# Kernel tuning notes

Hardware: AMD Instinct MI355X
Metric: run time of the kernel (lower is better)

## Reference

```python
import jax, jax.numpy as jnp
import numpy as np

ALPHA = 32.0
LN_EPS = 1e-5

def _cdist(a, b):
    # a: [C, M, K], b: [C, N, K] -> [C, M, N] euclidean distances
    d2 = (jnp.sum(a * a, -1)[:, :, None]
          + jnp.sum(b * b, -1)[:, None, :]
          - 2.0 * jnp.einsum('cmk,cnk->cmn', a, b))
    return jnp.sqrt(jnp.maximum(d2, 1e-12))

def setup_inputs() -> dict:
    key = jax.random.key(0)
    k1, k2 = jax.random.split(key)
    B, D, H, W, C = 8, 16, 28, 28, 256
    CN, SS = 128, 28 * 28
    x = jax.random.normal(k1, (B, D, H, W, C), dtype=jnp.float32)
    ln_weight = jnp.ones((C,), dtype=jnp.float32)
    ln_bias = jnp.zeros((C,), dtype=jnp.float32)
    cluster_center = jax.random.uniform(k2, (C, CN, SS), dtype=jnp.float32)
    return {"x": x, "ln_weight": ln_weight, "ln_bias": ln_bias,
            "cluster_center": cluster_center}

def reference(x, ln_weight, ln_bias, cluster_center):
    B, D, H, W, C = x.shape
    CN = cluster_center.shape[1]
    # LayerNorm over last dim (feature_dim)
    mu = jnp.mean(x, -1, keepdims=True)
    var = jnp.mean(jnp.square(x - mu), -1, keepdims=True)
    xn = (x - mu) * jax.lax.rsqrt(var + LN_EPS) * ln_weight + ln_bias
    # B D H W C -> C (B D) (H W)
    x_re = jnp.transpose(xn, (4, 0, 1, 2, 3)).reshape(C, B * D, H * W)
    soft_assign = _cdist(x_re, cluster_center)          # [C, B*D, CN]
    # C (B D) CN -> B D C CN
    x_distance = jnp.transpose(soft_assign.reshape(C, B, D, CN), (1, 2, 0, 3))
    # NegSoftAssign: exp(-alpha*(x - min)) normalized == softmax(-alpha*x)
    x_distance_assign = jax.nn.softmax(-ALPHA * x_distance, axis=-1)
    cluster_dist = _cdist(cluster_center, cluster_center)  # [C, CN, CN]
    return (x_distance, x_distance_assign, cluster_dist)
```

## Files before the change

### kernel.cpp

```cpp
#include <hip/hip_runtime.h>
#include <hip/hip_bf16.h>
#include <math.h>

#define C_DIM 256
#define BD    128
#define HW    784
#define CN    128
#define KPAD  832
#define KTILES 26

typedef short bf16x8 __attribute__((ext_vector_type(8)));
typedef float f32x4 __attribute__((ext_vector_type(4)));

__device__ inline ushort f2b(float f) {
  unsigned u = __float_as_uint(f);
  unsigned r = (u + 0x7FFFu + ((u >> 16) & 1u)) >> 16;
  return (ushort)r;
}

__global__ __launch_bounds__(256) void ln_transpose_kernel(
    const float* __restrict__ x, const float* __restrict__ lnw,
    const float* __restrict__ lnb, ushort* __restrict__ xre,
    float* __restrict__ anorm) {
  __shared__ ushort btile[256 * 64];
  __shared__ float nbuf[4][256];
  const int t = threadIdx.x, bd = blockIdx.y, bx = blockIdx.x;
  const int hw0 = bx * 64;
  const int w = t >> 6, lane = t & 63;
  const int q = lane >> 4, l = lane & 15;
  const bool last = (bx == 12);
  const int ngroups = last ? 1 : 4;
  const int rpw = ngroups * 4;
  if (last) {
    for (int r = 16; r < 64; r += 4)
      *(ushort4*)&btile[t * 64 + r] = make_ushort4(0, 0, 0, 0);
  }
  float4 wv[4], bv[4];
  for (int s = 0; s < 4; ++s) {
    wv[s] = *(const float4*)(lnw + s * 64 + l * 4);
    bv[s] = *(const float4*)(lnb + s * 64 + l * 4);
  }
  float nrm[4][4];
  for (int s = 0; s < 4; ++s)
    for (int j = 0; j < 4; ++j) nrm[s][j] = 0.f;
  const float* xb = x + ((size_t)bd * HW + hw0) * 256 + l * 4;
  const int xr = l & 12;
  for (int g = 0; g < ngroups; ++g) {
    int r = w * rpw + g * 4 + q;
    float4 v[4];
    for (int s = 0; s < 4; ++s)
      v[s] = *(const float4*)(xb + (size_t)r * 256 + s * 64);
    float sum = 0.f, sq = 0.f;
    for (int s = 0; s < 4; ++s) {
      sum += v[s].x + v[s].y + v[s].z + v[s].w;
      sq = fmaf(v[s].x, v[s].x, sq); sq = fmaf(v[s].y, v[s].y, sq);
      sq = fmaf(v[s].z, v[s].z, sq); sq = fmaf(v[s].w, v[s].w, sq);
    }
    for (int off = 1; off <= 8; off <<= 1) {
      sum += __shfl_xor(sum, off, 64);
      sq  += __shfl_xor(sq, off, 64);
    }
    float mu = sum * (1.f / 256.f);
    float var = fmaf(-mu, mu, sq * (1.f / 256.f));
    float sc = rsqrtf(var + 1e-5f);
    int rp = r ^ xr;
    for (int s = 0; s < 4; ++s) {
      float y0 = (v[s].x - mu) * sc * wv[s].x + bv[s].x;
      float y1 = (v[s].y - mu) * sc * wv[s].y + bv[s].y;
      float y2 = (v[s].z - mu) * sc * wv[s].z + bv[s].z;
      float y3 = (v[s].w - mu) * sc * wv[s].w + bv[s].w;
      nrm[s][0] = fmaf(y0, y0, nrm[s][0]);
      nrm[s][1] = fmaf(y1, y1, nrm[s][1]);
      nrm[s][2] = fmaf(y2, y2, nrm[s][2]);
      nrm[s][3] = fmaf(y3, y3, nrm[s][3]);
      int c = s * 64 + l * 4;
      btile[(c + 0) * 64 + rp] = f2b(y0);
      btile[(c + 1) * 64 + rp] = f2b(y1);
      btile[(c + 2) * 64 + rp] = f2b(y2);
      btile[(c + 3) * 64 + rp] = f2b(y3);
    }
  }
  for (int s = 0; s < 4; ++s)
    for (int j = 0; j < 4; ++j) {
      float v = nrm[s][j];
      v += __shfl_xor(v, 16, 64);
      v += __shfl_xor(v, 32, 64);
      nrm[s][j] = v;
    }
  if (q == 0)
    for (int s = 0; s < 4; ++s)
      for (int j = 0; j < 4; ++j) nbuf[w][s * 64 + l * 4 + j] = nrm[s][j];
  __syncthreads();
  float tot = nbuf[0][t] + nbuf[1][t] + nbuf[2][t] + nbuf[3][t];
  atomicAdd(&anorm[t * 128 + bd], tot);
  for (int i = 0; i < 16; ++i) {
    int c = w * 64 + i * 4 + (lane >> 4);
    int xw = (w * 16 + i) & 12;
    int ho = (lane & 15) * 4;
    uint2 val = *(const uint2*)&btile[c * 64 + (ho ^ xw)];
    *(uint2*)(xre + (size_t)c * (BD * KPAD) + (size_t)bd * KPAD + hw0 + ho) = val;
  }
}

__global__ __launch_bounds__(256) void cc_convert_kernel(
    const float* __restrict__ cc, ushort* __restrict__ ccb,
    float* __restrict__ bnorm) {
  int b = blockIdx.x, c = b >> 3;
  int t = threadIdx.x, w = t >> 6, lane = t & 63;
  int q = lane >> 4, l = lane & 15;
  int r = (b & 7) * 16 + w * 4 + q;
  const float4* src = (const float4*)(cc + ((size_t)c * CN + r) * HW);
  ushort* dst = ccb + ((size_t)c * CN + r) * KPAD;
  float nrm = 0.f;
  for (int i = 0; i < 13; ++i) {
    int f = i * 16 + l;
    if (f < 196) {
      float4 v = src[f];
      nrm = fmaf(v.x, v.x, nrm); nrm = fmaf(v.y, v.y, nrm);
      nrm = fmaf(v.z, v.z, nrm); nrm = fmaf(v.w, v.w, nrm);
      ushort4 o; o.x = f2b(v.x); o.y = f2b(v.y); o.z = f2b(v.z); o.w = f2b(v.w);
      *(ushort4*)(dst + f * 4) = o;
    }
  }
  for (int off = 1; off <= 8; off <<= 1) nrm += __shfl_xor(nrm, off, 64);
  if (l == 0) bnorm[c * 128 + r] = nrm;
  if (l < 12) *(ushort4*)(dst + 784 + l * 4) = make_ushort4(0, 0, 0, 0);
}

__global__ __launch_bounds__(256, 4) void gemm_mfma_kernel(
    const ushort* __restrict__ xre, const ushort* __restrict__ ccb,
    const float* __restrict__ anorm, const float* __restrict__ bnorm,
    float* __restrict__ out_d, float* __restrict__ out_c) {
  __shared__ __align__(16) ushort At[2][4096];
  __shared__ __align__(16) ushort Bt[2][2048];
  const int bx = blockIdx.x;
  const int c = bx >> 2, mode = (bx >> 1) & 1, nh = bx & 1;
  const int t = threadIdx.x, w = t >> 6, lane = t & 63;
  const int quad = lane >> 4, ln = lane & 15;
  const ushort* Ag = (mode ? ccb : xre) + (size_t)c * (128 * KPAD);
  const ushort* Bg = ccb + (size_t)c * (128 * KPAD) + (size_t)(nh * 64) * KPAD;

  f32x4 acc[2][4];
  for (int i = 0; i < 2; ++i)
    for (int j = 0; j < 4; ++j) acc[i][j] = f32x4{0.f, 0.f, 0.f, 0.f};

  const int ciA0 = w * 128 + lane, ciA1 = ciA0 + 64;
  const int rowA0 = ciA0 >> 2, rowA1 = ciA1 >> 2;
  const int qA0 = (ciA0 & 3) ^ (rowA0 & 3), qA1 = (ciA1 & 3) ^ (rowA1 & 3);
  const ushort* gA0 = Ag + (size_t)rowA0 * KPAD + qA0 * 8;
  const ushort* gA1 = Ag + (size_t)rowA1 * KPAD + qA1 * 8;
  const int rowB = t >> 2, qB = (t & 3) ^ (rowB & 3);
  const ushort* gB = Bg + (size_t)rowB * KPAD + qB * 8;

#define ISSUE(k, p)                                                            \
  do {                                                                         \
    int kb = (k) * 32;                                                         \
    __builtin_amdgcn_global_load_lds(                                          \
        (const __attribute__((address_space(1))) unsigned int*)(gA0 + kb),     \
        (__attribute__((address_space(3))) unsigned int*)&At[p][ciA0 * 8], 16, 0, 0); \
    __builtin_amdgcn_global_load_lds(                                          \
        (const __attribute__((address_space(1))) unsigned int*)(gA1 + kb),     \
        (__attribute__((address_space(3))) unsigned int*)&At[p][ciA1 * 8], 16, 0, 0); \
    if (!mode)                                                                 \
      __builtin_amdgcn_global_load_lds(                                        \
          (const __attribute__((address_space(1))) unsigned int*)(gB + kb),    \
          (__attribute__((address_space(3))) unsigned int*)&Bt[p][t * 8], 16, 0, 0); \
  } while (0)

  ISSUE(0, 0);
  for (int k0 = 0; k0 < KTILES; ++k0) {
    __syncthreads();
    if (k0 < KTILES - 1) ISSUE(k0 + 1, (k0 + 1) & 1);
    const int p = k0 & 1;
    const ushort* Ab = At[p];
    bf16x8 af[2], bf[4];
    for (int i = 0; i < 2; ++i) {
      int m = w * 32 + i * 16 + ln;
      af[i] = *(const bf16x8*)&Ab[(m * 4 + (quad ^ (m & 3))) * 8];
    }
    for (int j = 0; j < 4; ++j) {
      int n = j * 16 + ln;
      if (mode) {
        int mr = nh * 64 + n;
        bf[j] = *(const bf16x8*)&Ab[(mr * 4 + (quad ^ (mr & 3))) * 8];
      } else {
        bf[j] = *(const bf16x8*)&Bt[p][(n * 4 + (quad ^ (n & 3))) * 8];
      }
    }
    for (int i = 0; i < 2; ++i)
      for (int j = 0; j < 4; ++j)
        acc[i][j] = __builtin_amdgcn_mfma_f32_16x16x32_bf16(af[i], bf[j], acc[i][j], 0, 0, 0);
  }
#undef ISSUE

  const float* rn = (mode ? bnorm : anorm) + c * 128;
  const float* cnp = bnorm + c * 128 + nh * 64;
  float cnv[4];
  for (int j = 0; j < 4; ++j) cnv[j] = cnp[j * 16 + ln];
  for (int i = 0; i < 2; ++i) {
    float rv[4];
    for (int r = 0; r < 4; ++r) rv[r] = rn[w * 32 + i * 16 + quad * 4 + r];
    for (int r = 0; r < 4; ++r) {
      int m = w * 32 + i * 16 + quad * 4 + r;
      float dr[4];
      for (int j = 0; j < 4; ++j) {
        float d2 = rv[r] + cnv[j] - 2.f * acc[i][j][r];
        dr[j] = sqrtf(fmaxf(d2, 1e-12f));
      }
      if (mode) {
        float* ob = out_c + (size_t)c * (128 * 128) + (size_t)m * 128 + nh * 64;
        for (int j = 0; j < 4; ++j) ob[j * 16 + ln] = dr[j];
      } else {
        float* ob = out_d + ((size_t)m * 256 + c) * 128 + nh * 64;
        for (int j = 0; j < 4; ++j) ob[j * 16 + ln] = dr[j];
      }
    }
  }
}

__global__ __launch_bounds__(256) void softmax_kernel(
    const float* __restrict__ out_d, float* __restrict__ out_s) {
  const int t = threadIdx.x, w = t >> 6, lane = t & 63;
  const int q = lane >> 4, l = lane & 15;
  const int row = blockIdx.x * 16 + w * 4 + q;
  const float4* src = (const float4*)(out_d + (size_t)row * 128);
  float4 v0 = src[l], v1 = src[l + 16];
  float mn = fminf(fminf(fminf(v0.x, v0.y), fminf(v0.z, v0.w)),
                   fminf(fminf(v1.x, v1.y), fminf(v1.z, v1.w)));
  for (int off = 1; off <= 8; off <<= 1) mn = fminf(mn, __shfl_xor(mn, off, 64));
  float e[8];
  e[0] = __expf(-32.f * (v0.x - mn)); e[1] = __expf(-32.f * (v0.y - mn));
  e[2] = __expf(-32.f * (v0.z - mn)); e[3] = __expf(-32.f * (v0.w - mn));
  e[4] = __expf(-32.f * (v1.x - mn)); e[5] = __expf(-32.f * (v1.y - mn));
  e[6] = __expf(-32.f * (v1.z - mn)); e[7] = __expf(-32.f * (v1.w - mn));
  float s = e[0] + e[1] + e[2] + e[3] + e[4] + e[5] + e[6] + e[7];
  for (int off = 1; off <= 8; off <<= 1) s += __shfl_xor(s, off, 64);
  float inv = 1.f / s;
  float4* dst = (float4*)(out_s + (size_t)row * 128);
  dst[l]      = make_float4(e[0] * inv, e[1] * inv, e[2] * inv, e[3] * inv);
  dst[l + 16] = make_float4(e[4] * inv, e[5] * inv, e[6] * inv, e[7] * inv);
}

extern "C" void kernel_launch(void* const* d_in, const int* in_sizes, int n_in,
                              void* d_out, int out_size, void* d_ws, size_t ws_size,
                              hipStream_t stream) {
  const float* x   = (const float*)d_in[0];
  const float* lnw = (const float*)d_in[1];
  const float* lnb = (const float*)d_in[2];
  const float* cc  = (const float*)d_in[3];
  float* out   = (float*)d_out;
  float* out_d = out;
  float* out_s = out + 4194304;
  float* out_c = out + 8388608;

  ushort* xre_b = (ushort*)d_ws;
  ushort* cc_b  = xre_b + 27262976;
  float*  anorm = (float*)(cc_b + 27262976);
  float*  bnorm = anorm + 32768;

  hipMemsetAsync(anorm, 0, 32768 * sizeof(float), stream);
  ln_transpose_kernel<<<dim3(13, 128), 256, 0, stream>>>(x, lnw, lnb, xre_b, anorm);
  cc_convert_kernel<<<2048, 256, 0, stream>>>(cc, cc_b, bnorm);
  gemm_mfma_kernel<<<1024, 256, 0, stream>>>(xre_b, cc_b, anorm, bnorm, out_d, out_c);
  softmax_kernel<<<2048, 256, 0, stream>>>(out_d, out_s);
}
```

Measured before the change: 315.3 us.

## Fuse softmax into GEMM epilogue and share cluster-center tiles per channel

Replaces the four-block-per-channel GEMM with one 512-thread block per channel. That block computes both the x-to-center distances and the center-to-center distances from a single shared B tile, reusing the B fragment as the A operand for the center GEMM. The softmax is folded into the epilogue, since each wave holds full 128-wide rows, which removes the separate softmax kernel and its reread of out_d. The trade-off is only 256 blocks, which lowers occupancy and parallelism, and more accumulator registers per thread.

```diff
diff --git a/kernel.cpp b/kernel.cpp
--- a/kernel.cpp
+++ b/kernel.cpp
@@ -127,44 +127,38 @@
   if (l < 12) *(ushort4*)(dst + 784 + l * 4) = make_ushort4(0, 0, 0, 0);
 }
 
-__global__ __launch_bounds__(256, 4) void gemm_mfma_kernel(
+__global__ __launch_bounds__(512) void gemm_fused_kernel(
     const ushort* __restrict__ xre, const ushort* __restrict__ ccb,
     const float* __restrict__ anorm, const float* __restrict__ bnorm,
-    float* __restrict__ out_d, float* __restrict__ out_c) {
+    float* __restrict__ out_d, float* __restrict__ out_s,
+    float* __restrict__ out_c) {
   __shared__ __align__(16) ushort At[2][4096];
-  __shared__ __align__(16) ushort Bt[2][2048];
-  const int bx = blockIdx.x;
-  const int c = bx >> 2, mode = (bx >> 1) & 1, nh = bx & 1;
+  __shared__ __align__(16) ushort Bt[2][4096];
+  const int c = blockIdx.x;
   const int t = threadIdx.x, w = t >> 6, lane = t & 63;
   const int quad = lane >> 4, ln = lane & 15;
-  const ushort* Ag = (mode ? ccb : xre) + (size_t)c * (128 * KPAD);
-  const ushort* Bg = ccb + (size_t)c * (128 * KPAD) + (size_t)(nh * 64) * KPAD;
-
-  f32x4 acc[2][4];
-  for (int i = 0; i < 2; ++i)
-    for (int j = 0; j < 4; ++j) acc[i][j] = f32x4{0.f, 0.f, 0.f, 0.f};
-
-  const int ciA0 = w * 128 + lane, ciA1 = ciA0 + 64;
-  const int rowA0 = ciA0 >> 2, rowA1 = ciA1 >> 2;
-  const int qA0 = (ciA0 & 3) ^ (rowA0 & 3), qA1 = (ciA1 & 3) ^ (rowA1 & 3);
-  const ushort* gA0 = Ag + (size_t)rowA0 * KPAD + qA0 * 8;
-  const ushort* gA1 = Ag + (size_t)rowA1 * KPAD + qA1 * 8;
-  const int rowB = t >> 2, qB = (t & 3) ^ (rowB & 3);
-  const ushort* gB = Bg + (size_t)rowB * KPAD + qB * 8;
+  const ushort* Ag = xre + (size_t)c * (128 * KPAD);
+  const ushort* Bg = ccb + (size_t)c * (128 * KPAD);
+
+  f32x4 accx[8], accc[8];
+  for (int j = 0; j < 8; ++j) {
+    accx[j] = f32x4{0.f, 0.f, 0.f, 0.f};
+    accc[j] = f32x4{0.f, 0.f, 0.f, 0.f};
+  }
+
+  const int srow = t >> 2, scq = (t & 3) ^ (srow & 3);
+  const ushort* gA = Ag + (size_t)srow * KPAD + scq * 8;
+  const ushort* gB = Bg + (size_t)srow * KPAD + scq * 8;
 
 #define ISSUE(k, p)                                                            \
   do {                                                                         \
     int kb = (k) * 32;                                                         \
     __builtin_amdgcn_global_load_lds(                                          \
-        (const __attribute__((address_space(1))) unsigned int*)(gA0 + kb),     \
-        (__attribute__((address_space(3))) unsigned int*)&At[p][ciA0 * 8], 16, 0, 0); \
+        (const __attribute__((address_space(1))) unsigned int*)(gA + kb),      \
+        (__attribute__((address_space(3))) unsigned int*)&At[p][t * 8], 16, 0, 0); \
     __builtin_amdgcn_global_load_lds(                                          \
-        (const __attribute__((address_space(1))) unsigned int*)(gA1 + kb),     \
-        (__attribute__((address_space(3))) unsigned int*)&At[p][ciA1 * 8], 16, 0, 0); \
-    if (!mode)                                                                 \
-      __builtin_amdgcn_global_load_lds(                                        \
-          (const __attribute__((address_space(1))) unsigned int*)(gB + kb),    \
-          (__attribute__((address_space(3))) unsigned int*)&Bt[p][t * 8], 16, 0, 0); \
+        (const __attribute__((address_space(1))) unsigned int*)(gB + kb),      \
+        (__attribute__((address_space(3))) unsigned int*)&Bt[p][t * 8], 16, 0, 0); \
   } while (0)
 
   ISSUE(0, 0);
@@ -172,73 +166,58 @@
     __syncthreads();
     if (k0 < KTILES - 1) ISSUE(k0 + 1, (k0 + 1) & 1);
     const int p = k0 & 1;
-    const ushort* Ab = At[p];
-    bf16x8 af[2], bf[4];
-    for (int i = 0; i < 2; ++i) {
-      int m = w * 32 + i * 16 + ln;
-      af[i] = *(const bf16x8*)&Ab[(m * 4 + (quad ^ (m & 3))) * 8];
-    }
-    for (int j = 0; j < 4; ++j) {
+    const int m = w * 16 + ln;
+    bf16x8 af = *(const bf16x8*)&At[p][(m * 4 + (quad ^ (m & 3))) * 8];
+    bf16x8 bf[8];
+    for (int j = 0; j < 8; ++j) {
       int n = j * 16 + ln;
-      if (mode) {
-        int mr = nh * 64 + n;
-        bf[j] = *(const bf16x8*)&Ab[(mr * 4 + (quad ^ (mr & 3))) * 8];
-      } else {
-        bf[j] = *(const bf16x8*)&Bt[p][(n * 4 + (quad ^ (n & 3))) * 8];
-      }
-    }
-    for (int i = 0; i < 2; ++i)
-      for (int j = 0; j < 4; ++j)
-        acc[i][j] = __builtin_amdgcn_mfma_f32_16x16x32_bf16(af[i], bf[j], acc[i][j], 0, 0, 0);
+      bf[j] = *(const bf16x8*)&Bt[p][(n * 4 + (quad ^ (n & 3))) * 8];
+    }
+    bf16x8 ar = bf[w];
+    for (int j = 0; j < 8; ++j) {
+      accx[j] = __builtin_amdgcn_mfma_f32_16x16x32_bf16(af, bf[j], accx[j], 0, 0, 0);
+      accc[j] = __builtin_amdgcn_mfma_f32_16x16x32_bf16(ar, bf[j], accc[j], 0, 0, 0);
+    }
   }
 #undef ISSUE
 
-  const float* rn = (mode ? bnorm : anorm) + c * 128;
-  const float* cnp = bnorm + c * 128 + nh * 64;
-  float cnv[4];
-  for (int j = 0; j < 4; ++j) cnv[j] = cnp[j * 16 + ln];
-  for (int i = 0; i < 2; ++i) {
-    float rv[4];
-    for (int r = 0; r < 4; ++r) rv[r] = rn[w * 32 + i * 16 + quad * 4 + r];
-    for (int r = 0; r < 4; ++r) {
-      int m = w * 32 + i * 16 + quad * 4 + r;
-      float dr[4];
-      for (int j = 0; j < 4; ++j) {
-        float d2 = rv[r] + cnv[j] - 2.f * acc[i][j][r];
-        dr[j] = sqrtf(fmaxf(d2, 1e-12f));
-      }
-      if (mode) {
-        float* ob = out_c + (size_t)c * (128 * 128) + (size_t)m * 128 + nh * 64;
-        for (int j = 0; j < 4; ++j) ob[j * 16 + ln] = dr[j];
-      } else {
-        float* ob = out_d + ((size_t)m * 256 + c) * 128 + nh * 64;
-        for (int j = 0; j < 4; ++j) ob[j * 16 + ln] = dr[j];
-      }
-    }
-  }
-}
-
-__global__ __launch_bounds__(256) void softmax_kernel(
-    const float* __restrict__ out_d, float* __restrict__ out_s) {
-  const int t = threadIdx.x, w = t >> 6, lane = t & 63;
-  const int q = lane >> 4, l = lane & 15;
-  const int row = blockIdx.x * 16 + w * 4 + q;
-  const float4* src = (const float4*)(out_d + (size_t)row * 128);
-  float4 v0 = src[l], v1 = src[l + 16];
-  float mn = fminf(fminf(fminf(v0.x, v0.y), fminf(v0.z, v0.w)),
-                   fminf(fminf(v1.x, v1.y), fminf(v1.z, v1.w)));
-  for (int off = 1; off <= 8; off <<= 1) mn = fminf(mn, __shfl_xor(mn, off, 64));
-  float e[8];
-  e[0] = __expf(-32.f * (v0.x - mn)); e[1] = __expf(-32.f * (v0.y - mn));
-  e[2] = __expf(-32.f * (v0.z - mn)); e[3] = __expf(-32.f * (v0.w - mn));
-  e[4] = __expf(-32.f * (v1.x - mn)); e[5] = __expf(-32.f * (v1.y - mn));
-  e[6] = __expf(-32.f * (v1.z - mn)); e[7] = __expf(-32.f * (v1.w - mn));
-  float s = e[0] + e[1] + e[2] + e[3] + e[4] + e[5] + e[6] + e[7];
-  for (int off = 1; off <= 8; off <<= 1) s += __shfl_xor(s, off, 64);
-  float inv = 1.f / s;
-  float4* dst = (float4*)(out_s + (size_t)row * 128);
-  dst[l]      = make_float4(e[0] * inv, e[1] * inv, e[2] * inv, e[3] * inv);
-  dst[l + 16] = make_float4(e[4] * inv, e[5] * inv, e[6] * inv, e[7] * inv);
+  const float* an = anorm + c * 128;
+  const float* bn = bnorm + c * 128;
+  float cn[8];
+  for (int j = 0; j < 8; ++j) cn[j] = bn[j * 16 + ln];
+  float rx[4], rc[4];
+  for (int r = 0; r < 4; ++r) {
+    int m = w * 16 + quad * 4 + r;
+    rx[r] = an[m];
+    rc[r] = bn[m];
+  }
+  for (int r = 0; r < 4; ++r) {
+    int m = w * 16 + quad * 4 + r;
+    float* ob = out_c + (size_t)c * (128 * 128) + (size_t)m * 128;
+    for (int j = 0; j < 8; ++j) {
+      float d2 = rc[r] + cn[j] - 2.f * accc[j][r];
+      ob[j * 16 + ln] = sqrtf(fmaxf(d2, 1e-12f));
+    }
+  }
+  for (int r = 0; r < 4; ++r) {
+    int m = w * 16 + quad * 4 + r;
+    float dr[8];
+    for (int j = 0; j < 8; ++j) {
+      float d2 = rx[r] + cn[j] - 2.f * accx[j][r];
+      dr[j] = sqrtf(fmaxf(d2, 1e-12f));
+    }
+    float* ob = out_d + ((size_t)m * 256 + c) * 128;
+    for (int j = 0; j < 8; ++j) ob[j * 16 + ln] = dr[j];
+    float mn = dr[0];
+    for (int j = 1; j < 8; ++j) mn = fminf(mn, dr[j]);
+    for (int off = 1; off <= 8; off <<= 1) mn = fminf(mn, __shfl_xor(mn, off, 64));
+    float e[8], s = 0.f;
+    for (int j = 0; j < 8; ++j) { e[j] = __expf(-32.f * (dr[j] - mn)); s += e[j]; }
+    for (int off = 1; off <= 8; off <<= 1) s += __shfl_xor(s, off, 64);
+    float inv = 1.f / s;
+    float* os = out_s + ((size_t)m * 256 + c) * 128;
+    for (int j = 0; j < 8; ++j) os[j * 16 + ln] = e[j] * inv;
+  }
 }
 
 extern "C" void kernel_launch(void* const* d_in, const int* in_sizes, int n_in,
@@ -261,6 +240,6 @@
   hipMemsetAsync(anorm, 0, 32768 * sizeof(float), stream);
   ln_transpose_kernel<<<dim3(13, 128), 256, 0, stream>>>(x, lnw, lnb, xre_b, anorm);
   cc_convert_kernel<<<2048, 256, 0, stream>>>(cc, cc_b, bnorm);
-  gemm_mfma_kernel<<<1024, 256, 0, stream>>>(xre_b, cc_b, anorm, bnorm, out_d, out_c);
-  softmax_kernel<<<2048, 256, 0, stream>>>(out_d, out_s);
-}
+  gemm_fused_kernel<<<256, 512, 0, stream>>>(xre_b, cc_b, anorm, bnorm,
+                                             out_d, out_s, out_c);
+}
```

Result: slower. 492.7 us (+56.3%).
